# Optimization experiments

Hardware: AMD Instinct MI355X
Metric: run time of the kernel (lower is better)

The kernel has to match this reference:

```python
import jax, jax.numpy as jnp
import numpy as np
import math

N_HEAD = 16

def setup_inputs() -> dict:
    key = jax.random.key(0)
    k1, k2, k3, k4, k5 = jax.random.split(key, 5)
    B, T, C = 8, 1024, 1024
    scale = 0.02
    return {
        "x": jax.random.normal(k1, (B, T, C), dtype=jnp.float32),
        "w_attn": jax.random.normal(k2, (C, 3 * C), dtype=jnp.float32) * scale,
        "b_attn": jax.random.normal(k3, (3 * C,), dtype=jnp.float32) * scale,
        "w_proj": jax.random.normal(k4, (C, C), dtype=jnp.float32) * scale,
        "b_proj": jax.random.normal(k5, (C,), dtype=jnp.float32) * scale,
    }

def reference(x, w_attn, b_attn, w_proj, b_proj):
    B, T, C = x.shape
    H = N_HEAD
    hd = C // H
    # QKV projection: [B,T,3C]
    qkv = jnp.einsum("btc,cd->btd", x, w_attn) + b_attn
    q, k, v = jnp.split(qkv, 3, axis=-1)
    # [B,T,C] -> [B,H,T,hd]
    def heads(t):
        return t.reshape(B, T, H, hd).transpose(0, 2, 1, 3)
    q, k, v = heads(q), heads(k), heads(v)
    # scaled QK^T: [B,H,T,T]
    att = jnp.einsum("bhqd,bhkd->bhqk", q, k) * (1.0 / math.sqrt(hd))
    # causal mask (tril of block_size cropped to T)
    causal = jnp.tril(jnp.ones((T, T), dtype=bool))
    att = jnp.where(causal, att, jnp.float32(-jnp.inf))
    att = jax.nn.softmax(att, axis=-1)
    # attention-weighted values: [B,H,T,hd] -> [B,T,C]
    y = jnp.einsum("bhqk,bhkd->bhqd", att, v)
    y = y.transpose(0, 2, 1, 3).reshape(B, T, C)
    # output projection
    return jnp.einsum("btc,cd->btd", y, w_proj) + b_proj
```

## Files before the change

### kernel.cpp

```cpp
#include <hip/hip_runtime.h>

typedef __bf16 bf16x8 __attribute__((ext_vector_type(8)));
typedef float f32x4 __attribute__((ext_vector_type(4)));
typedef unsigned short u16;
typedef unsigned int u32;

__device__ __forceinline__ u16 f2bf(float f) {
  u32 u = __builtin_bit_cast(u32, f);
  u32 r = (u + 0x7FFFu + ((u >> 16) & 1u)) >> 16;
  return (u16)r;
}

__device__ __forceinline__ void gload_lds16(const u16* g, u16* l) {
  __builtin_amdgcn_global_load_lds(
      (const __attribute__((address_space(1))) u32*)g,
      (__attribute__((address_space(3))) u32*)l, 16, 0, 0);
}

__global__ void cast_x_kernel(const float* __restrict__ in, u16* __restrict__ out, int n4) {
  int i = blockIdx.x * blockDim.x + threadIdx.x;
  if (i >= n4) return;
  float4 v = ((const float4*)in)[i];
  uint2 o;
  o.x = (u32)f2bf(v.x) | ((u32)f2bf(v.y) << 16);
  o.y = (u32)f2bf(v.z) | ((u32)f2bf(v.w) << 16);
  ((uint2*)out)[i] = o;
}

__global__ void transpose_cast_kernel(const float* __restrict__ in, u16* __restrict__ out,
                                      int K, int N) {
  __shared__ float tile[32][33];
  int n0 = blockIdx.x * 32, k0 = blockIdx.y * 32;
  int tx = threadIdx.x & 31, ty = threadIdx.x >> 5;
#pragma unroll
  for (int i = 0; i < 32; i += 8)
    tile[ty + i][tx] = in[(size_t)(k0 + ty + i) * N + n0 + tx];
  __syncthreads();
#pragma unroll
  for (int i = 0; i < 32; i += 8)
    out[(size_t)(n0 + ty + i) * K + k0 + tx] = f2bf(tile[tx][ty + i]);
}

template <int MODE>
__global__ __launch_bounds__(256, 3) void gemm_bf16(
    const u16* __restrict__ A, const u16* __restrict__ Bt,
    const float* __restrict__ bias, u16* __restrict__ out_q,
    float* __restrict__ out_f, int M, int N, int K) {
  __shared__ alignas(16) u16 As[128 * 32];
  __shared__ alignas(16) u16 Bs[128 * 32];
  const int tiles_n = N >> 7;
  const int tm = (int)blockIdx.x / tiles_n;
  const int tn = (int)blockIdx.x % tiles_n;
  const int tid = threadIdx.x;
  const int wave = tid >> 6, lane = tid & 63;
  const int wr = (wave >> 1) * 64, wc = (wave & 1) * 64;
  const int lr = lane & 15, lg = lane >> 4;

  f32x4 acc[4][4] = {};
  const size_t a_base = (size_t)(tm * 128) * K;
  const size_t b_base = (size_t)(tn * 128) * K;

  for (int k0 = 0; k0 < K; k0 += 32) {
#pragma unroll
    for (int i = 0; i < 2; ++i) {
      int flat = i * 256 + tid;
      int row = flat >> 2, ch = flat & 3;
      int sw = (ch ^ (row & 3)) * 8;
      gload_lds16(A + a_base + (size_t)row * K + k0 + sw, &As[flat * 8]);
      gload_lds16(Bt + b_base + (size_t)row * K + k0 + sw, &Bs[flat * 8]);
    }
    __syncthreads();
    bf16x8 af[4], bfr[4];
#pragma unroll
    for (int m = 0; m < 4; ++m) {
      int row = wr + m * 16 + lr;
      af[m] = *(const bf16x8*)&As[row * 32 + ((lg ^ (row & 3)) * 8)];
    }
#pragma unroll
    for (int n = 0; n < 4; ++n) {
      int row = wc + n * 16 + lr;
      bfr[n] = *(const bf16x8*)&Bs[row * 32 + ((lg ^ (row & 3)) * 8)];
    }
#pragma unroll
    for (int m = 0; m < 4; ++m)
#pragma unroll
      for (int n = 0; n < 4; ++n)
        acc[m][n] = __builtin_amdgcn_mfma_f32_16x16x32_bf16(af[m], bfr[n], acc[m][n], 0, 0, 0);
    __syncthreads();
  }

  const int row0 = tm * 128 + wr;
  const int col0 = tn * 128 + wc;
#pragma unroll
  for (int n = 0; n < 4; ++n) {
    int col = col0 + n * 16 + lr;
    float bv = bias[col];
#pragma unroll
    for (int m = 0; m < 4; ++m) {
#pragma unroll
      for (int r = 0; r < 4; ++r) {
        int mrow = row0 + m * 16 + lg * 4 + r;
        float v = acc[m][n][r] + bv;
        if constexpr (MODE == 0) {
          int which = col >> 10, c = col & 1023;
          int h = c >> 6, d = c & 63;
          int b = mrow >> 10, t = mrow & 1023;
          out_q[(size_t)which * 8388608 + ((((size_t)b * 16 + h) * 1024 + t) << 6) + d] = f2bf(v);
        } else {
          out_f[(size_t)mrow * N + col] = v;
        }
      }
    }
  }
}

__global__ __launch_bounds__(256, 2) void attn_kernel(
    const u16* __restrict__ Qb, const u16* __restrict__ Kb,
    const u16* __restrict__ Vb, u16* __restrict__ yb) {
  __shared__ alignas(16) u16 Ks[64 * 64];
  __shared__ alignas(16) u16 Vt[64 * 64];
  __shared__ alignas(16) u16 Pl[4][32 * 64];
  __shared__ float abuf[4][32];

  const int bid = blockIdx.x;
  const int xcd = bid & 7, j = bid >> 3;
  const int bh = ((j >> 2) << 3) + xcd;
  const int pr = j & 3;
  const size_t hb = (size_t)bh * 65536;
  const int tid = threadIdx.x, w = tid >> 6, lane = tid & 63;
  const int lr = lane & 15, lg = lane >> 4;
  const int b = bh >> 4, h = bh & 15;

  for (int pass = 0; pass < 2; ++pass) {
    const int qt = pass ? (7 - pr) : pr;
    const int q0 = qt * 128 + w * 32;

    bf16x8 qf[2][2];
#pragma unroll
    for (int mi = 0; mi < 2; ++mi)
#pragma unroll
      for (int ks = 0; ks < 2; ++ks)
        qf[mi][ks] = *(const bf16x8*)&Qb[hb + (size_t)(q0 + mi * 16 + lr) * 64 + ks * 32 + lg * 8];

    float m_run[2] = {-1e30f, -1e30f}, l_run[2] = {0.f, 0.f};
    f32x4 o[2][4] = {};

    const int nkt = (qt + 1) * 2;
    for (int kt = 0; kt < nkt; ++kt) {
#pragma unroll
      for (int i = 0; i < 2; ++i) {
        int flat = i * 256 + tid;
        int row = flat >> 3, ch = flat & 7;
        gload_lds16(Kb + hb + (size_t)(kt * 64 + row) * 64 + ((ch ^ (row & 7)) * 8), &Ks[flat * 8]);
      }
      {
        int key = tid & 63, d0 = (tid >> 6) * 16;
        const u16* src = Vb + hb + (size_t)(kt * 64 + key) * 64 + d0;
        union { uint4 v[2]; u16 s[16]; } tmp;
        tmp.v[0] = *(const uint4*)src;
        tmp.v[1] = *(const uint4*)(src + 8);
#pragma unroll
        for (int jj = 0; jj < 16; ++jj) {
          int d = d0 + jj;
          Vt[d * 64 + (key ^ ((d & 7) << 3))] = tmp.s[jj];
        }
      }
      __syncthreads();

      if (kt * 64 <= q0 + 31) {
        f32x4 s[4][2] = {};
        __builtin_amdgcn_s_setprio(1);
#pragma unroll
        for (int ni = 0; ni < 4; ++ni) {
          int krow = ni * 16 + lr;
          bf16x8 kf0 = *(const bf16x8*)&Ks[krow * 64 + ((lg ^ (krow & 7)) * 8)];
          bf16x8 kf1 = *(const bf16x8*)&Ks[krow * 64 + (((4 + lg) ^ (krow & 7)) * 8)];
#pragma unroll
          for (int mi = 0; mi < 2; ++mi) {
            s[ni][mi] = __builtin_amdgcn_mfma_f32_16x16x32_bf16(kf0, qf[mi][0], s[ni][mi], 0, 0, 0);
            s[ni][mi] = __builtin_amdgcn_mfma_f32_16x16x32_bf16(kf1, qf[mi][1], s[ni][mi], 0, 0, 0);
          }
        }
        __builtin_amdgcn_s_setprio(0);

        const bool need_mask = (kt * 64 + 63) > q0;
        float alpha_l[2];
#pragma unroll
        for (int mi = 0; mi < 2; ++mi) {
          float v = -1e30f;
#pragma unroll
          for (int ni = 0; ni < 4; ++ni)
#pragma unroll
            for (int r = 0; r < 4; ++r) {
              float sv = s[ni][mi][r];
              if (need_mask) {
                int ka = kt * 64 + ni * 16 + lg * 4 + r;
                int qa = q0 + mi * 16 + lr;
                if (ka > qa) sv = -1e30f;
              }
              s[ni][mi][r] = sv;
              v = fmaxf(v, sv);
            }
          v = fmaxf(v, __shfl_xor(v, 16));
          v = fmaxf(v, __shfl_xor(v, 32));
          float mn = fmaxf(m_run[mi], v);
          float al = __expf((m_run[mi] - mn) * 0.125f);
          m_run[mi] = mn;
          float mh = mn * 0.125f;
          float rs = 0.f;
#pragma unroll
          for (int ni = 0; ni < 4; ++ni)
#pragma unroll
            for (int r = 0; r < 4; ++r) {
              float p = __expf(s[ni][mi][r] * 0.125f - mh);
              s[ni][mi][r] = p;
              rs += p;
            }
          rs += __shfl_xor(rs, 16);
          rs += __shfl_xor(rs, 32);
          l_run[mi] = l_run[mi] * al + rs;
          alpha_l[mi] = al;
        }
        if (lg == 0) {
          abuf[w][lr] = alpha_l[0];
          abuf[w][16 + lr] = alpha_l[1];
        }
#pragma unroll
        for (int mi = 0; mi < 2; ++mi) {
          int qrow = mi * 16 + lr;
          u16* dst = &Pl[w][qrow * 64];
          int sw = (qrow & 7) << 3;
#pragma unroll
          for (int ni = 0; ni < 4; ++ni)
#pragma unroll
            for (int r = 0; r < 4; ++r)
              dst[(ni * 16 + lg * 4 + r) ^ sw] = f2bf(s[ni][mi][r]);
        }
        asm volatile("s_waitcnt lgkmcnt(0)" ::: "memory");
#pragma unroll
        for (int mi = 0; mi < 2; ++mi) {
          f32x4 av;
#pragma unroll
          for (int r = 0; r < 4; ++r) av[r] = abuf[w][mi * 16 + lg * 4 + r];
#pragma unroll
          for (int nd = 0; nd < 4; ++nd)
#pragma unroll
            for (int r = 0; r < 4; ++r) o[mi][nd][r] *= av[r];
        }
        __builtin_amdgcn_s_setprio(1);
#pragma unroll
        for (int ks = 0; ks < 2; ++ks) {
          bf16x8 pf[2];
#pragma unroll
          for (int mi = 0; mi < 2; ++mi) {
            int prow = mi * 16 + lr;
            pf[mi] = *(const bf16x8*)&Pl[w][prow * 64 + (((ks * 4 + lg) ^ (prow & 7)) * 8)];
          }
#pragma unroll
          for (int nd = 0; nd < 4; ++nd) {
            int vrow = nd * 16 + lr;
            bf16x8 vf = *(const bf16x8*)&Vt[vrow * 64 + (((ks * 4 + lg) ^ (vrow & 7)) * 8)];
#pragma unroll
            for (int mi = 0; mi < 2; ++mi)
              o[mi][nd] = __builtin_amdgcn_mfma_f32_16x16x32_bf16(pf[mi], vf, o[mi][nd], 0, 0, 0);
          }
        }
        __builtin_amdgcn_s_setprio(0);
      }
      __syncthreads();
    }

    if (lg == 0) {
      abuf[w][lr] = l_run[0];
      abuf[w][16 + lr] = l_run[1];
    }
    asm volatile("s_waitcnt lgkmcnt(0)" ::: "memory");
#pragma unroll
    for (int mi = 0; mi < 2; ++mi) {
      f32x4 inv;
#pragma unroll
      for (int r = 0; r < 4; ++r) inv[r] = 1.f / abuf[w][mi * 16 + lg * 4 + r];
#pragma unroll
      for (int nd = 0; nd < 4; ++nd)
#pragma unroll
        for (int r = 0; r < 4; ++r) {
          int t = q0 + mi * 16 + lg * 4 + r;
          int c = h * 64 + nd * 16 + lr;
          yb[((size_t)b * 1024 + t) * 1024 + c] = f2bf(o[mi][nd][r] * inv[r]);
        }
    }
    __syncthreads();
  }
}

extern "C" void kernel_launch(void* const* d_in, const int* in_sizes, int n_in,
                              void* d_out, int out_size, void* d_ws, size_t ws_size,
                              hipStream_t stream) {
  const float* x = (const float*)d_in[0];
  const float* w_attn = (const float*)d_in[1];
  const float* b_attn = (const float*)d_in[2];
  const float* w_proj = (const float*)d_in[3];
  const float* b_proj = (const float*)d_in[4];
  float* out = (float*)d_out;

  u16* ws = (u16*)d_ws;
  u16* xb = ws;
  u16* watT = xb + 8388608;
  u16* wpT = watT + 3145728;
  u16* Qb = wpT + 1048576;
  u16* yb = xb;

  cast_x_kernel<<<8192, 256, 0, stream>>>(x, xb, 2097152);
  {
    dim3 g(96, 32);
    transpose_cast_kernel<<<g, 256, 0, stream>>>(w_attn, watT, 1024, 3072);
  }
  {
    dim3 g(32, 32);
    transpose_cast_kernel<<<g, 256, 0, stream>>>(w_proj, wpT, 1024, 1024);
  }
  gemm_bf16<0><<<64 * 24, 256, 0, stream>>>(xb, watT, b_attn, Qb, nullptr, 8192, 3072, 1024);
  attn_kernel<<<512, 256, 0, stream>>>(Qb, Qb + 8388608, Qb + 2 * 8388608, yb);
  gemm_bf16<1><<<64 * 8, 256, 0, stream>>>(yb, wpT, b_proj, nullptr, out, 8192, 1024, 1024);
}
```

Before: 170.8 us.

## Add 256x256 double-buffered QKV GEMM with XCD-aware block swizzle

Replaces the 128x128 QKV projection GEMM with a new 256x256-tile, 512-thread kernel that stages K=64 chunks through double-buffered LDS. Global-to-LDS loads for the next tiles are interleaved with four MFMA quadrant phases, and waves get raised priority during MFMA runs. The aim is more operand reuse per LDS byte and hiding global load latency. It also adds a blockIdx swizzle that maps consecutive tiles onto the same XCD, applied to the old GEMM as well for better L2 locality. In exchange, the larger tile gives only 384 blocks, which may fill the CUs unevenly, and the kernel uses 128KB of LDS per block.

```diff
diff --git a/kernel.cpp b/kernel.cpp
--- a/kernel.cpp
+++ b/kernel.cpp
@@ -42,6 +42,159 @@
 }
 
 template <int MODE>
+__global__ __launch_bounds__(512, 2) void gemm256(
+    const u16* __restrict__ A, const u16* __restrict__ Bt,
+    const float* __restrict__ bias, u16* __restrict__ out_q,
+    float* __restrict__ out_f, int M, int N, int K) {
+  __shared__ alignas(16) u16 lds[2][2][256 * 64];
+  const int tiles_n = N >> 8;
+  const int bid = blockIdx.x;
+  const int cpx = (int)gridDim.x >> 3;
+  const int swz = (bid & 7) * cpx + (bid >> 3);
+  const int tm = swz / tiles_n, tn = swz % tiles_n;
+  const int tid = threadIdx.x, lane = tid & 63;
+  const int w = tid >> 6, wm = w >> 2, wn = w & 3;
+  const int lr = lane & 15, lg = lane >> 4;
+  const int NT = K >> 6;
+
+  f32x4 acc[2][2][4][2] = {};
+
+  auto stage = [&](int t, int which) {
+    const int isB = which & 1, half = which >> 1;
+    const u16* mat = isB ? Bt : A;
+    const int row0 = (isB ? tn : tm) * 256 + half * 128;
+    u16* lbase = &lds[t & 1][isB][half * 8192];
+#pragma unroll
+    for (int j = 0; j < 2; ++j) {
+      int c = tid + j * 512;
+      int lc = c ^ ((c >> 3) & 3);
+      int row = lc >> 3, k8 = lc & 7;
+      gload_lds16(mat + (size_t)(row0 + row) * K + t * 64 + k8 * 8, lbase + c * 8);
+    }
+  };
+  auto rdA = [&](int cur, int mh, int m, int kk) -> bf16x8 {
+    int row = mh * 128 + wm * 64 + m * 16 + lr;
+    int e = (row * 64 + kk * 32 + lg * 8) ^ ((row & 3) << 3);
+    return *(const bf16x8*)&lds[cur][0][e];
+  };
+  auto rdB = [&](int cur, int nh, int n, int kk) -> bf16x8 {
+    int row = nh * 128 + wn * 32 + n * 16 + lr;
+    int e = (row * 64 + kk * 32 + lg * 8) ^ ((row & 3) << 3);
+    return *(const bf16x8*)&lds[cur][1][e];
+  };
+
+  stage(0, 0); stage(0, 1); stage(0, 2); stage(0, 3);
+  stage(1, 0); stage(1, 1); stage(1, 2);
+  asm volatile("s_waitcnt vmcnt(6)" ::: "memory");
+  __builtin_amdgcn_s_barrier();
+
+  bf16x8 af[4][2], b0[2][2], b1[2][2];
+  for (int t = 0; t < NT; ++t) {
+    const int cur = t & 1;
+#pragma unroll
+    for (int m = 0; m < 4; ++m)
+#pragma unroll
+      for (int kk = 0; kk < 2; ++kk) af[m][kk] = rdA(cur, 0, m, kk);
+#pragma unroll
+    for (int n = 0; n < 2; ++n)
+#pragma unroll
+      for (int kk = 0; kk < 2; ++kk) b0[n][kk] = rdB(cur, 0, n, kk);
+    if (t + 1 < NT) stage(t + 1, 3);
+    __builtin_amdgcn_s_barrier();
+    asm volatile("s_waitcnt lgkmcnt(0)" ::: "memory");
+    __builtin_amdgcn_sched_barrier(0);
+    __builtin_amdgcn_s_setprio(1);
+#pragma unroll
+    for (int m = 0; m < 4; ++m)
+#pragma unroll
+      for (int n = 0; n < 2; ++n)
+#pragma unroll
+        for (int kk = 0; kk < 2; ++kk)
+          acc[0][0][m][n] = __builtin_amdgcn_mfma_f32_16x16x32_bf16(af[m][kk], b0[n][kk], acc[0][0][m][n], 0, 0, 0);
+    __builtin_amdgcn_s_setprio(0);
+    __builtin_amdgcn_s_barrier();
+#pragma unroll
+    for (int n = 0; n < 2; ++n)
+#pragma unroll
+      for (int kk = 0; kk < 2; ++kk) b1[n][kk] = rdB(cur, 1, n, kk);
+    if (t + 2 < NT) stage(t + 2, 0);
+    __builtin_amdgcn_s_barrier();
+    asm volatile("s_waitcnt lgkmcnt(0)" ::: "memory");
+    __builtin_amdgcn_sched_barrier(0);
+    __builtin_amdgcn_s_setprio(1);
+#pragma unroll
+    for (int m = 0; m < 4; ++m)
+#pragma unroll
+      for (int n = 0; n < 2; ++n)
+#pragma unroll
+        for (int kk = 0; kk < 2; ++kk)
+          acc[0][1][m][n] = __builtin_amdgcn_mfma_f32_16x16x32_bf16(af[m][kk], b1[n][kk], acc[0][1][m][n], 0, 0, 0);
+    __builtin_amdgcn_s_setprio(0);
+    __builtin_amdgcn_s_barrier();
+#pragma unroll
+    for (int m = 0; m < 4; ++m)
+#pragma unroll
+      for (int kk = 0; kk < 2; ++kk) af[m][kk] = rdA(cur, 1, m, kk);
+    if (t + 2 < NT) stage(t + 2, 1);
+    __builtin_amdgcn_s_barrier();
+    asm volatile("s_waitcnt lgkmcnt(0)" ::: "memory");
+    __builtin_amdgcn_sched_barrier(0);
+    __builtin_amdgcn_s_setprio(1);
+#pragma unroll
+    for (int m = 0; m < 4; ++m)
+#pragma unroll
+      for (int n = 0; n < 2; ++n)
+#pragma unroll
+        for (int kk = 0; kk < 2; ++kk)
+          acc[1][0][m][n] = __builtin_amdgcn_mfma_f32_16x16x32_bf16(af[m][kk], b0[n][kk], acc[1][0][m][n], 0, 0, 0);
+    __builtin_amdgcn_s_setprio(0);
+    __builtin_amdgcn_s_barrier();
+    if (t + 2 < NT) stage(t + 2, 2);
+    __builtin_amdgcn_s_barrier();
+    __builtin_amdgcn_s_setprio(1);
+#pragma unroll
+    for (int m = 0; m < 4; ++m)
+#pragma unroll
+      for (int n = 0; n < 2; ++n)
+#pragma unroll
+        for (int kk = 0; kk < 2; ++kk)
+          acc[1][1][m][n] = __builtin_amdgcn_mfma_f32_16x16x32_bf16(af[m][kk], b1[n][kk], acc[1][1][m][n], 0, 0, 0);
+    __builtin_amdgcn_s_setprio(0);
+    if (t + 2 < NT) {
+      asm volatile("s_waitcnt vmcnt(6)" ::: "memory");
+    } else {
+      asm volatile("s_waitcnt vmcnt(0)" ::: "memory");
+    }
+    __builtin_amdgcn_s_barrier();
+  }
+
+#pragma unroll
+  for (int mh = 0; mh < 2; ++mh)
+#pragma unroll
+    for (int nh = 0; nh < 2; ++nh)
+#pragma unroll
+      for (int n = 0; n < 2; ++n) {
+        int col = tn * 256 + nh * 128 + wn * 32 + n * 16 + lr;
+        float bv = bias[col];
+#pragma unroll
+        for (int m = 0; m < 4; ++m)
+#pragma unroll
+          for (int r = 0; r < 4; ++r) {
+            int mrow = tm * 256 + mh * 128 + wm * 64 + m * 16 + lg * 4 + r;
+            float v = acc[mh][nh][m][n][r] + bv;
+            if constexpr (MODE == 0) {
+              int which = col >> 10, c = col & 1023;
+              int h = c >> 6, d = c & 63;
+              int b = mrow >> 10, tq = mrow & 1023;
+              out_q[(size_t)which * 8388608 + ((((size_t)b * 16 + h) * 1024 + tq) << 6) + d] = f2bf(v);
+            } else {
+              out_f[(size_t)mrow * N + col] = v;
+            }
+          }
+      }
+}
+
+template <int MODE>
 __global__ __launch_bounds__(256, 3) void gemm_bf16(
     const u16* __restrict__ A, const u16* __restrict__ Bt,
     const float* __restrict__ bias, u16* __restrict__ out_q,
@@ -49,8 +202,11 @@
   __shared__ alignas(16) u16 As[128 * 32];
   __shared__ alignas(16) u16 Bs[128 * 32];
   const int tiles_n = N >> 7;
-  const int tm = (int)blockIdx.x / tiles_n;
-  const int tn = (int)blockIdx.x % tiles_n;
+  const int bid0 = blockIdx.x;
+  const int cpx = (int)gridDim.x >> 3;
+  const int swz = (bid0 & 7) * cpx + (bid0 >> 3);
+  const int tm = swz / tiles_n;
+  const int tn = swz % tiles_n;
   const int tid = threadIdx.x;
   const int wave = tid >> 6, lane = tid & 63;
   const int wr = (wave >> 1) * 64, wc = (wave & 1) * 64;
@@ -319,7 +475,7 @@
     dim3 g(32, 32);
     transpose_cast_kernel<<<g, 256, 0, stream>>>(w_proj, wpT, 1024, 1024);
   }
-  gemm_bf16<0><<<64 * 24, 256, 0, stream>>>(xb, watT, b_attn, Qb, nullptr, 8192, 3072, 1024);
+  gemm256<0><<<32 * 12, 512, 0, stream>>>(xb, watT, b_attn, Qb, nullptr, 8192, 3072, 1024);
   attn_kernel<<<512, 256, 0, stream>>>(Qb, Qb + 8388608, Qb + 2 * 8388608, yb);
   gemm_bf16<1><<<64 * 8, 256, 0, stream>>>(yb, wpT, b_proj, nullptr, out, 8192, 1024, 1024);
 }
```

After: 174.5 us. +2.2%, slower.

## Remap GEMM blocks per XCD, strengthen LDS swizzle, vectorize QKV epilogue stores

Applied to the files above, without the earlier changes.

Remaps GEMM block indices so consecutive tiles land on the same XCD, which should improve L2 reuse of A/B panels. The LDS XOR swizzle gains an extra row-based term to cut bank conflicts on the fragment reads. For the QKV GEMM, swapping the MFMA operands transposes the accumulator layout, so each lane holds 4 consecutive head-dim values. The epilogue can then write them as one packed 8-byte bf16 store with a float4 bias load, replacing scattered 2-byte stores. The block remap assumes the grid size is divisible by 8.

```diff
diff --git a/kernel.cpp b/kernel.cpp
--- a/kernel.cpp
+++ b/kernel.cpp
@@ -49,8 +49,11 @@
   __shared__ alignas(16) u16 As[128 * 32];
   __shared__ alignas(16) u16 Bs[128 * 32];
   const int tiles_n = N >> 7;
-  const int tm = (int)blockIdx.x / tiles_n;
-  const int tn = (int)blockIdx.x % tiles_n;
+  const int bid0 = blockIdx.x;
+  const int cpx = (int)gridDim.x >> 3;
+  const int swz = (bid0 & 7) * cpx + (bid0 >> 3);
+  const int tm = swz / tiles_n;
+  const int tn = swz % tiles_n;
   const int tid = threadIdx.x;
   const int wave = tid >> 6, lane = tid & 63;
   const int wr = (wave >> 1) * 64, wc = (wave & 1) * 64;
@@ -65,7 +68,7 @@
     for (int i = 0; i < 2; ++i) {
       int flat = i * 256 + tid;
       int row = flat >> 2, ch = flat & 3;
-      int sw = (ch ^ (row & 3)) * 8;
+      int sw = (ch ^ (row & 3) ^ ((row >> 2) & 3)) * 8;
       gload_lds16(A + a_base + (size_t)row * K + k0 + sw, &As[flat * 8]);
       gload_lds16(Bt + b_base + (size_t)row * K + k0 + sw, &Bs[flat * 8]);
     }
@@ -74,42 +77,60 @@
 #pragma unroll
     for (int m = 0; m < 4; ++m) {
       int row = wr + m * 16 + lr;
-      af[m] = *(const bf16x8*)&As[row * 32 + ((lg ^ (row & 3)) * 8)];
+      af[m] = *(const bf16x8*)&As[row * 32 + ((lg ^ (row & 3) ^ ((row >> 2) & 3)) * 8)];
     }
 #pragma unroll
     for (int n = 0; n < 4; ++n) {
       int row = wc + n * 16 + lr;
-      bfr[n] = *(const bf16x8*)&Bs[row * 32 + ((lg ^ (row & 3)) * 8)];
+      bfr[n] = *(const bf16x8*)&Bs[row * 32 + ((lg ^ (row & 3) ^ ((row >> 2) & 3)) * 8)];
     }
 #pragma unroll
     for (int m = 0; m < 4; ++m)
 #pragma unroll
-      for (int n = 0; n < 4; ++n)
-        acc[m][n] = __builtin_amdgcn_mfma_f32_16x16x32_bf16(af[m], bfr[n], acc[m][n], 0, 0, 0);
+      for (int n = 0; n < 4; ++n) {
+        if constexpr (MODE == 0)
+          acc[m][n] = __builtin_amdgcn_mfma_f32_16x16x32_bf16(bfr[n], af[m], acc[m][n], 0, 0, 0);
+        else
+          acc[m][n] = __builtin_amdgcn_mfma_f32_16x16x32_bf16(af[m], bfr[n], acc[m][n], 0, 0, 0);
+      }
     __syncthreads();
   }
 
-  const int row0 = tm * 128 + wr;
-  const int col0 = tn * 128 + wc;
-#pragma unroll
-  for (int n = 0; n < 4; ++n) {
-    int col = col0 + n * 16 + lr;
-    float bv = bias[col];
-#pragma unroll
-    for (int m = 0; m < 4; ++m) {
-#pragma unroll
-      for (int r = 0; r < 4; ++r) {
-        int mrow = row0 + m * 16 + lg * 4 + r;
-        float v = acc[m][n][r] + bv;
-        if constexpr (MODE == 0) {
-          int which = col >> 10, c = col & 1023;
-          int h = c >> 6, d = c & 63;
-          int b = mrow >> 10, t = mrow & 1023;
-          out_q[(size_t)which * 8388608 + ((((size_t)b * 16 + h) * 1024 + t) << 6) + d] = f2bf(v);
-        } else {
-          out_f[(size_t)mrow * N + col] = v;
-        }
-      }
+  if constexpr (MODE == 0) {
+    const int tok0 = tm * 128 + wr;
+    const int col0 = tn * 128 + wc;
+#pragma unroll
+    for (int n = 0; n < 4; ++n) {
+      int ncol = col0 + n * 16 + lg * 4;
+      float4 bv = *(const float4*)&bias[ncol];
+      int which = ncol >> 10, c = ncol & 1023;
+      int h = c >> 6, d = c & 63;
+#pragma unroll
+      for (int m = 0; m < 4; ++m) {
+        int tok = tok0 + m * 16 + lr;
+        int b = tok >> 10, t = tok & 1023;
+        union { u16 s[4]; uint2 v; } pk;
+        pk.s[0] = f2bf(acc[m][n][0] + bv.x);
+        pk.s[1] = f2bf(acc[m][n][1] + bv.y);
+        pk.s[2] = f2bf(acc[m][n][2] + bv.z);
+        pk.s[3] = f2bf(acc[m][n][3] + bv.w);
+        *(uint2*)&out_q[(size_t)which * 8388608 + ((((size_t)b * 16 + h) * 1024 + t) << 6) + d] = pk.v;
+      }
+    }
+  } else {
+    const int row0 = tm * 128 + wr;
+    const int col0 = tn * 128 + wc;
+#pragma unroll
+    for (int n = 0; n < 4; ++n) {
+      int col = col0 + n * 16 + lr;
+      float bv = bias[col];
+#pragma unroll
+      for (int m = 0; m < 4; ++m)
+#pragma unroll
+        for (int r = 0; r < 4; ++r) {
+          int mrow = row0 + m * 16 + lg * 4 + r;
+          out_f[(size_t)mrow * N + col] = acc[m][n][r] + bv;
+        }
     }
   }
 }
```

Measured after the change: 171.4 us. No clear change (+0.4%).
